# Performance work log

Measured on AMD Instinct MI355X. Metric: run time of the kernel, lower is better.

Reference implementation:

```python
import jax, jax.numpy as jnp
import numpy as np
from jax import lax

RATIO = 0.25
K = 16
EPS = 1e-5
B, N, CX, COUT, CAUX = 16, 4096, 64, 128, 32


def _fps(p, m):
    # Farthest point sampling on one cloud p:(N,3); deterministic start at index 0.
    mind = jnp.sum((p - p[0]) ** 2, axis=-1)  # (N,) min sq-dist to selected set
    def step(mind, _):
        nxt = jnp.argmax(mind)
        d = jnp.sum((p - p[nxt]) ** 2, axis=-1)
        return jnp.minimum(mind, d), nxt
    _, rest = lax.scan(step, mind, None, length=m - 1)
    return jnp.concatenate([jnp.zeros((1,), jnp.int32), rest.astype(jnp.int32)])


def setup_inputs() -> dict:
    key = jax.random.key(0)
    k1, k2, k3, k4, k5, k6 = jax.random.split(key, 6)
    P = B * N
    x = jax.random.normal(k1, (P, CX), jnp.float32)
    pos = jax.random.normal(k2, (P, 3), jnp.float32)
    batch = jnp.repeat(jnp.arange(B, dtype=jnp.int32), N)  # equal-size clouds
    aux = jax.random.normal(k3, (P, CAUX), jnp.float32)
    # MLP params: Linear(CX->COUT) + BatchNorm affine
    W = jax.random.normal(k4, (CX, COUT), jnp.float32) * (1.0 / np.sqrt(CX))
    b = jax.random.normal(k5, (COUT,), jnp.float32) * 0.02
    gamma = jnp.ones((COUT,), jnp.float32) + 0.1 * jax.random.normal(k6, (COUT,), jnp.float32)
    beta = jnp.zeros((COUT,), jnp.float32)
    return {"x": x, "pos": pos, "batch": batch, "aux": aux,
            "W": W, "b": b, "gamma": gamma, "beta": beta}


def reference(x, pos, batch, aux, W, b, gamma, beta):
    P = x.shape[0]
    nb = int(batch[-1]) + 1            # number of clouds (equal-size)
    n = P // nb
    m = int(n * RATIO)                 # clusters per cloud
    pos_b = pos.reshape(nb, n, 3)
    # --- FPS per cloud ---
    idx_local = jax.vmap(lambda p: _fps(p, m))(pos_b)                     # (B, M)
    id_clusters = (idx_local + jnp.arange(nb, dtype=jnp.int32)[:, None] * n).reshape(-1)
    centers = jnp.take_along_axis(pos_b, idx_local[..., None], axis=1)    # (B, M, 3)
    # --- kNN of all points to cluster centers, within each cloud ---
    d2 = jnp.sum((centers[:, :, None, :] - pos_b[:, None, :, :]) ** 2, axis=-1)  # (B, M, N)
    _, nb_local = lax.top_k(-d2, K)                                       # (B, M, K)
    nb_global = (nb_local + jnp.arange(nb, dtype=jnp.int32)[:, None, None] * n).reshape(-1)
    # --- MLP: Linear -> BatchNorm(batch stats, train mode) -> ReLU ---
    h = x @ W + b
    mu = jnp.mean(h, axis=0)
    var = jnp.var(h, axis=0)
    x_trans = jax.nn.relu(gamma * (h - mu) * lax.rsqrt(var + EPS) + beta)  # (P, Cout)
    # --- gather + per-cluster max / mean pooling (== scatter over knn edges) ---
    x_out = jnp.max(x_trans[nb_global].reshape(nb * m, K, -1), axis=1)     # (B*M, Cout)
    aux_out = jnp.mean(aux[nb_global].reshape(nb * m, K, -1), axis=1)      # (B*M, Caux)
    sub_pos = centers.reshape(-1, 3)
    sub_batch = batch[id_clusters]
    return x_out, sub_pos, sub_batch, aux_out, id_clusters
```

## Files before the change

kernel.cpp:

```cpp
#include <hip/hip_runtime.h>
#include <hip/hip_bf16.h>
#include <math.h>

#define NB    16
#define NPC   4096
#define MPC   1024
#define PTOT  65536
#define NCLU  16384
#define KNN_  16
#define CIN   64
#define COUT_ 128
#define CAUX_ 32

#define OFF_XOUT   0
#define OFF_SUBPOS (NCLU*COUT_)
#define OFF_SUBB   (OFF_SUBPOS + NCLU*3)
#define OFF_AUX    (OFF_SUBB + NCLU)
#define OFF_IDCL   (OFF_AUX + NCLU*CAUX_)

#define WS_H        0
#define WS_CENTERS  (PTOT*COUT_*4)
#define WS_STATS    (WS_CENTERS + NCLU*16)
#define WS_NEED     (WS_STATS + 256*4)

#define SM_LX    0
#define SM_LY    16384
#define SM_LZ    32768
#define SM_CAND  49152
#define SM_CSEL  49664
#define SM_SIDX  53760
#define SM_HIST  70144
#define SM_SCANA 72192
#define SM_SCANB 74240
#define SM_XT    0
#define SM_WL    17408
#define SM_BS    50176
#define SM_BQ    50688
#define SM_SIZE  76288

__device__ __forceinline__ double dmax(double a, double b) { return __builtin_fmax(a, b); }
__device__ __forceinline__ double dmin(double a, double b) { return __builtin_fmin(a, b); }
__device__ __forceinline__ double pk(float d, int lo) {
  return __hiloint2double(__float_as_int(d), lo);
}
__device__ __forceinline__ int pk_lo(double k) {
  return (int)(unsigned)(__double_as_longlong(k) & 0xFFFFFFFFll);
}

template <int CTRL>
__device__ __forceinline__ double dpp64(double v) {
  long long u = __double_as_longlong(v);
  int lo = (int)(unsigned)(u & 0xFFFFFFFFll);
  int hi = (int)(unsigned)((unsigned long long)u >> 32);
  int rlo = __builtin_amdgcn_update_dpp(0, lo, CTRL, 0xf, 0xf, true);
  int rhi = __builtin_amdgcn_update_dpp(0, hi, CTRL, 0xf, 0xf, true);
  return __longlong_as_double(((long long)rhi << 32) | (long long)(unsigned)rlo);
}
template <int CTRL>
__device__ __forceinline__ float dpp32(float x) {
  return __int_as_float(__builtin_amdgcn_update_dpp(0, __float_as_int(x), CTRL, 0xf, 0xf, true));
}
#define ROR1 0x121
#define ROR2 0x122
#define ROR4 0x124
#define ROR8 0x128

__device__ __forceinline__ double rowmax16(double w) {
  w = dmax(w, dpp64<ROR1>(w));
  w = dmax(w, dpp64<ROR2>(w));
  w = dmax(w, dpp64<ROR4>(w));
  w = dmax(w, dpp64<ROR8>(w));
  return w;
}
__device__ __forceinline__ float row16maxf(float m) {
  m = fmaxf(m, dpp32<ROR1>(m));
  m = fmaxf(m, dpp32<ROR2>(m));
  m = fmaxf(m, dpp32<ROR4>(m));
  m = fmaxf(m, dpp32<ROR8>(m));
  return m;
}
__device__ __forceinline__ float row16minf(float m) {
  m = fminf(m, dpp32<ROR1>(m));
  m = fminf(m, dpp32<ROR2>(m));
  m = fminf(m, dpp32<ROR4>(m));
  m = fminf(m, dpp32<ROR8>(m));
  return m;
}

__device__ __forceinline__ int mort3(int x, int y, int z) {
  int m = 0;
  #pragma unroll
  for (int bb = 0; bb < 3; ++bb)
    m |= (((x >> bb) & 1) << (3*bb + 2)) | (((y >> bb) & 1) << (3*bb + 1)) |
         (((z >> bb) & 1) << (3*bb));
  return m;
}

__device__ void fps_block(char* smem, const float* __restrict__ pos,
                          float4* __restrict__ centers, float* __restrict__ out)
{
  #pragma clang fp contract(off)
  float* lx = (float*)(smem + SM_LX);
  float* ly = (float*)(smem + SM_LY);
  float* lz = (float*)(smem + SM_LZ);
  double* cand = (double*)(smem + SM_CAND);
  int*   csel = (int*)(smem + SM_CSEL);
  int*   sidx = (int*)(smem + SM_SIDX);
  int*   hist = (int*)(smem + SM_HIST);
  float* bbs  = (float*)(smem + SM_HIST);
  int*   sA   = (int*)(smem + SM_SCANA);
  int*   sB   = (int*)(smem + SM_SCANB);
  const int b = blockIdx.x;
  const int t = threadIdx.x;
  const float* pb = pos + (size_t)b * NPC * 3;
  const int entry  = (t >> 6) * 4 + ((t >> 4) & 3);
  const bool writer = ((t & 15) == 0);

  float ox[8], oy[8], oz[8];
  {
    const float4* src = (const float4*)(pb + t * 24);
    float4 v[6];
    #pragma unroll
    for (int i = 0; i < 6; ++i) v[i] = src[i];
    const float* f = (const float*)v;
    #pragma unroll
    for (int j = 0; j < 8; ++j) {
      ox[j] = f[3*j]; oy[j] = f[3*j+1]; oz[j] = f[3*j+2];
      lx[t*8+j] = ox[j]; ly[t*8+j] = oy[j]; lz[t*8+j] = oz[j];
    }
  }
  float mnx = ox[0], mxx = ox[0], mny = oy[0], mxy = oy[0], mnz = oz[0], mxz = oz[0];
  #pragma unroll
  for (int j = 1; j < 8; ++j) {
    mnx = fminf(mnx, ox[j]); mxx = fmaxf(mxx, ox[j]);
    mny = fminf(mny, oy[j]); mxy = fmaxf(mxy, oy[j]);
    mnz = fminf(mnz, oz[j]); mxz = fmaxf(mxz, oz[j]);
  }
  mnx = row16minf(mnx); mxx = row16maxf(mxx);
  mny = row16minf(mny); mxy = row16maxf(mxy);
  mnz = row16minf(mnz); mxz = row16maxf(mxz);
  if (writer) {
    bbs[entry] = mnx; bbs[32+entry] = mxx; bbs[64+entry]  = mny;
    bbs[96+entry] = mxy; bbs[128+entry] = mnz; bbs[160+entry] = mxz;
  }
  __syncthreads();
  float gx0 = bbs[0], gx1 = bbs[32], gy0 = bbs[64], gy1 = bbs[96], gz0 = bbs[128], gz1 = bbs[160];
  #pragma unroll 8
  for (int w = 1; w < 32; ++w) {
    gx0 = fminf(gx0, bbs[w]);     gx1 = fmaxf(gx1, bbs[32+w]);
    gy0 = fminf(gy0, bbs[64+w]);  gy1 = fmaxf(gy1, bbs[96+w]);
    gz0 = fminf(gz0, bbs[128+w]); gz1 = fmaxf(gz1, bbs[160+w]);
  }
  __syncthreads();
  hist[t] = 0;
  __syncthreads();
  const float scx = 8.0f / ((gx1 - gx0) + 1e-6f);
  const float scy = 8.0f / ((gy1 - gy0) + 1e-6f);
  const float scz = 8.0f / ((gz1 - gz0) + 1e-6f);
  int key[8];
  #pragma unroll
  for (int j = 0; j < 8; ++j) {
    int cx = min(7, max(0, (int)((ox[j] - gx0) * scx)));
    int cy = min(7, max(0, (int)((oy[j] - gy0) * scy)));
    int cz = min(7, max(0, (int)((oz[j] - gz0) * scz)));
    key[j] = mort3(cx, cy, cz);
    atomicAdd(&hist[key[j]], 1);
  }
  __syncthreads();
  const int hv = hist[t];
  sA[t] = hv;
  __syncthreads();
  for (int off = 1; off < 512; off <<= 1) {
    const int o = (t >= off) ? sA[t - off] : 0;
    __syncthreads();
    sA[t] += o;
    __syncthreads();
  }
  sB[t] = sA[t] - hv;
  __syncthreads();
  #pragma unroll
  for (int j = 0; j < 8; ++j) {
    const int slot = atomicAdd(&sB[key[j]], 1);
    sidx[slot] = t*8 + j;
  }
  __syncthreads();
  float px[8], py[8], pz[8], mind[8];
  int lo8[8];
  float bxn = 1e30f, bxx = -1e30f, byn = 1e30f, byy = -1e30f, bzn = 1e30f, bzz = -1e30f;
  #pragma unroll
  for (int j = 0; j < 8; ++j) {
    const int sid = sidx[t*8 + j];
    px[j] = lx[sid]; py[j] = ly[sid]; pz[j] = lz[sid];
    lo8[j] = 4095 - sid;
    bxn = fminf(bxn, px[j]); bxx = fmaxf(bxx, px[j]);
    byn = fminf(byn, py[j]); byy = fmaxf(byy, py[j]);
    bzn = fminf(bzn, pz[j]); bzz = fmaxf(bzz, pz[j]);
  }
  const float x0 = lx[0], y0 = ly[0], z0 = lz[0];
  if (t == 0) csel[0] = 0;

  double bk;
  {
    double k4[4];
    #pragma unroll
    for (int jp = 0; jp < 4; ++jp) {
      const int j0 = 2*jp, j1 = 2*jp + 1;
      float dx0 = px[j0]-x0, dy0 = py[j0]-y0, dz0 = pz[j0]-z0;
      float dx1 = px[j1]-x0, dy1 = py[j1]-y0, dz1 = pz[j1]-z0;
      float d0 = (dx0*dx0 + dy0*dy0) + dz0*dz0;
      float d1 = (dx1*dx1 + dy1*dy1) + dz1*dz1;
      mind[j0] = d0; mind[j1] = d1;
      k4[jp] = dmax(pk(d0, lo8[j0]), pk(d1, lo8[j1]));
    }
    bk = dmax(dmax(k4[0], k4[1]), dmax(k4[2], k4[3]));
  }

  for (int s = 1; s < MPC; ++s) {
    double w = rowmax16(bk);
    const int ph = (s & 1) * 32;
    if (writer) cand[ph + entry] = w;
    __syncthreads();
    double2 pr = ((const double2*)(cand + ph))[t & 15];
    double w2 = rowmax16(dmax(pr.x, pr.y));
    const int sel = 4095 - pk_lo(w2);
    const float sx = lx[sel], sy = ly[sel], sz = lz[sel];
    if (t == 0) csel[s] = sel;
    const float bkhi = __int_as_float(__double2hiint(bk));
    const float cxd = fmaxf(fmaxf(bxn - sx, sx - bxx), 0.0f);
    const float cyd = fmaxf(fmaxf(byn - sy, sy - byy), 0.0f);
    const float czd = fmaxf(fmaxf(bzn - sz, sz - bzz), 0.0f);
    const float lb = 0.99f * ((cxd*cxd + cyd*cyd) + czd*czd);
    if (lb < bkhi) {
      double k4[4];
      #pragma unroll
      for (int jp = 0; jp < 4; ++jp) {
        const int j0 = 2*jp, j1 = 2*jp + 1;
        float dx0 = px[j0]-sx, dy0 = py[j0]-sy, dz0 = pz[j0]-sz;
        float dx1 = px[j1]-sx, dy1 = py[j1]-sy, dz1 = pz[j1]-sz;
        float d0 = (dx0*dx0 + dy0*dy0) + dz0*dz0;
        float d1 = (dx1*dx1 + dy1*dy1) + dz1*dz1;
        float m0 = fminf(mind[j0], d0), m1 = fminf(mind[j1], d1);
        mind[j0] = m0; mind[j1] = m1;
        k4[jp] = dmax(pk(m0, lo8[j0]), pk(m1, lo8[j1]));
      }
      bk = dmax(dmax(k4[0], k4[1]), dmax(k4[2], k4[3]));
    }
  }
  __syncthreads();
  for (int c = t; c < MPC; c += 512) {
    const int il = csel[c];
    const int cl = b*MPC + c;
    const float X = lx[il], Y = ly[il], Z = lz[il];
    centers[cl] = make_float4(X, Y, Z, 0.0f);
    out[OFF_SUBPOS + cl*3 + 0] = X;
    out[OFF_SUBPOS + cl*3 + 1] = Y;
    out[OFF_SUBPOS + cl*3 + 2] = Z;
    out[OFF_SUBB + cl] = (float)b;
    out[OFF_IDCL + cl] = (float)(b*NPC + il);
  }
}

__device__ void gemm_block(char* smem, const float* __restrict__ x,
                           const float* __restrict__ W, const float* __restrict__ bias,
                           float* __restrict__ h, float* __restrict__ stats, int blk)
{
  float (*xT)[68]  = (float(*)[68])(smem + SM_XT);
  float (*Wl)[128] = (float(*)[128])(smem + SM_WL);
  float* bsum = (float*)(smem + SM_BS);
  float* bsq  = (float*)(smem + SM_BQ);
  const int t = threadIdx.x;
  const int row0 = blk * 64;
  if (t < 128) { bsum[t] = 0.0f; bsq[t] = 0.0f; }
  #pragma unroll
  for (int i = 0; i < 8; ++i) {
    const int idx = t + i*512;
    xT[idx & 63][idx >> 6] = x[(size_t)row0*64 + idx];
  }
  #pragma unroll
  for (int i = 0; i < 16; ++i) {
    const int idx = t + i*512;
    ((float*)Wl)[idx] = W[idx];
  }
  __syncthreads();
  const int tx = t & 31, ty = t >> 5;
  float acc[4][4] = {};
  #pragma unroll 8
  for (int k = 0; k < 64; ++k) {
    const float4 a  = *(const float4*)&xT[k][ty*4];
    const float4 b0 = *(const float4*)&Wl[k][tx*4];
    const float av[4] = {a.x, a.y, a.z, a.w};
    const float bw[4] = {b0.x, b0.y, b0.z, b0.w};
    #pragma unroll
    for (int i2 = 0; i2 < 4; ++i2)
      #pragma unroll
      for (int e = 0; e < 4; ++e)
        acc[i2][e] += av[i2] * bw[e];
  }
  const int c0 = tx*4;
  float bb[4];
  #pragma unroll
  for (int e = 0; e < 4; ++e) bb[e] = bias[c0+e];
  float s4[4] = {}, q4[4] = {};
  #pragma unroll
  for (int i2 = 0; i2 < 4; ++i2) {
    float vv[4];
    #pragma unroll
    for (int e = 0; e < 4; ++e) {
      float v = acc[i2][e] + bb[e];
      vv[e] = v; s4[e] += v; q4[e] += v*v;
    }
    const int r = row0 + ty*4 + i2;
    *(float4*)&h[(size_t)r*128 + c0] = make_float4(vv[0], vv[1], vv[2], vv[3]);
  }
  #pragma unroll
  for (int e = 0; e < 4; ++e) {
    atomicAdd(&bsum[c0+e], s4[e]);
    atomicAdd(&bsq[c0+e],  q4[e]);
  }
  __syncthreads();
  if (t < 128) {
    atomicAdd(&stats[t],      bsum[t]);
    atomicAdd(&stats[128+t],  bsq[t]);
  }
}

__global__ __launch_bounds__(512) void fused_fps_gemm(const float* __restrict__ pos,
                                                      float4* __restrict__ centers,
                                                      float* __restrict__ out,
                                                      const float* __restrict__ x,
                                                      const float* __restrict__ W,
                                                      const float* __restrict__ bias,
                                                      float* __restrict__ h,
                                                      float* __restrict__ stats)
{
  __shared__ __align__(16) char smem[SM_SIZE];
  if (blockIdx.x < NB) fps_block(smem, pos, centers, out);
  else                 gemm_block(smem, x, W, bias, h, stats, blockIdx.x - NB);
}

#define KBIG __hiloint2double(0x7f7fffff, 0xffffffff)
#define CD_STRIDE 17

#define KP_CD    0
#define KP_SCL   69632
#define KP_SSH   70144
#define KP_FID   70656
#define KP_SIZE  72704

__global__ __launch_bounds__(512) void knn_pool(const float* __restrict__ pos,
                                                const float4* __restrict__ centers,
                                                const float* __restrict__ h,
                                                const float* __restrict__ aux,
                                                const float* __restrict__ stats,
                                                const float* __restrict__ gamma,
                                                const float* __restrict__ beta,
                                                float* __restrict__ out)
{
  #pragma clang fp contract(off)
  __shared__ __align__(16) char sm2[KP_SIZE];
  float4* lp = (float4*)(sm2);
  double* cd = (double*)(sm2 + KP_CD);
  float*  scl = (float*)(sm2 + KP_SCL);
  float*  ssh = (float*)(sm2 + KP_SSH);
  int*    fid = (int*)(sm2 + KP_FID);
  const int vblk = ((blockIdx.x & 7) << 6) | (blockIdx.x >> 3);
  const int b   = vblk >> 5;
  const int c0  = (vblk & 31) * 32;
  const int t   = threadIdx.x;
  const int q   = t & 15;
  const int cc  = t >> 4;
  if (t < 128) {
    const float inv = 1.0f / 65536.0f;
    const float mu  = stats[t] * inv;
    const float var = stats[128+t] * inv - mu*mu;
    const float sc  = gamma[t] * rsqrtf(var + 1e-5f);
    scl[t] = sc;
    ssh[t] = beta[t] - mu*sc;
  }
  const float* pb = pos + (size_t)b * NPC * 3;
  for (int i = t; i < NPC; i += 512)
    lp[i] = make_float4(pb[3*i], pb[3*i+1], pb[3*i+2], 0.0f);
  __syncthreads();
  const float4 C = centers[b*MPC + c0 + cc];
  double L[16];
  #pragma unroll
  for (int k = 0; k < 16; ++k) L[k] = KBIG;
  for (int jj = 0; jj < NPC/16; ++jj) {
    const int j = jj*16 + q;
    const float4 p = lp[j];
    float dx = C.x - p.x, dy = C.y - p.y, dz = C.z - p.z;
    float d2 = (dx*dx + dy*dy) + dz*dz;
    double nk = pk(d2, j);
    if (nk < L[0]) {
      #pragma unroll
      for (int k = 0; k < 15; ++k) L[k] = dmin(L[k], dmax(L[k+1], nk));
      L[15] = dmin(L[15], nk);
    }
  }
  __syncthreads();
  #pragma unroll
  for (int k = 0; k < 16; ++k) cd[t*CD_STRIDE + k] = L[k];
  __syncthreads();
  if (q < 4) {
    #pragma unroll
    for (int r = 1; r <= 3; ++r) {
      const double* src = cd + (cc*16 + q + 4*r)*CD_STRIDE;
      #pragma unroll
      for (int k = 0; k < 16; ++k) {
        double nk = src[k];
        if (nk < L[0]) {
          #pragma unroll
          for (int m = 0; m < 15; ++m) L[m] = dmin(L[m], dmax(L[m+1], nk));
          L[15] = dmin(L[15], nk);
        }
      }
    }
    #pragma unroll
    for (int k = 0; k < 16; ++k) cd[t*CD_STRIDE + k] = L[k];
  }
  __syncthreads();
  if (q == 0) {
    #pragma unroll
    for (int r = 1; r <= 3; ++r) {
      const double* src = cd + (cc*16 + r)*CD_STRIDE;
      #pragma unroll
      for (int k = 0; k < 16; ++k) {
        double nk = src[k];
        if (nk < L[0]) {
          #pragma unroll
          for (int m = 0; m < 15; ++m) L[m] = dmin(L[m], dmax(L[m+1], nk));
          L[15] = dmin(L[15], nk);
        }
      }
    }
    #pragma unroll
    for (int k = 0; k < 16; ++k) fid[cc*16 + k] = b*NPC + pk_lo(L[k]);
  }
  __syncthreads();
  for (int g = 0; g < 8; ++g) {
    const int cc2 = g*4 + (t >> 7);
    const int col = t & 127;
    const int cl  = b*MPC + c0 + cc2;
    const float sc = scl[col], sh = ssh[col];
    float mv = 0.0f;
    #pragma unroll
    for (int k = 0; k < 16; ++k) {
      const float hv = h[(size_t)fid[cc2*16 + k]*128 + col];
      mv = fmaxf(mv, fmaxf(sc*hv + sh, 0.0f));
    }
    out[OFF_XOUT + (size_t)cl*128 + col] = mv;
    if (col < 32) {
      float s = 0.0f;
      #pragma unroll
      for (int k = 0; k < 16; ++k) s += aux[(size_t)fid[cc2*16 + k]*32 + col];
      out[OFF_AUX + (size_t)cl*32 + col] = s * (1.0f/16.0f);
    }
  }
}

extern "C" void kernel_launch(void* const* d_in, const int* in_sizes, int n_in,
                              void* d_out, int out_size, void* d_ws, size_t ws_size,
                              hipStream_t stream)
{
  const float* x     = (const float*)d_in[0];
  const float* pos   = (const float*)d_in[1];
  const float* aux   = (const float*)d_in[3];
  const float* W     = (const float*)d_in[4];
  const float* bias  = (const float*)d_in[5];
  const float* gamma = (const float*)d_in[6];
  const float* beta  = (const float*)d_in[7];
  float* out = (float*)d_out;
  char*  ws  = (char*)d_ws;
  if (ws_size < (size_t)WS_NEED) return;

  float*  h       = (float*)(ws + WS_H);
  float4* centers = (float4*)(ws + WS_CENTERS);
  float*  stats   = (float*)(ws + WS_STATS);

  hipMemsetAsync(stats, 0, 256*4, stream);
  hipLaunchKernelGGL(fused_fps_gemm, dim3(NB + PTOT/64), dim3(512), 0, stream,
                     pos, centers, out, x, W, bias, h, stats);
  hipLaunchKernelGGL(knn_pool, dim3(512), dim3(512), 0, stream,
                     pos, centers, h, aux, stats, gamma, beta, out);
}
```

Before: 734.3 us.

## Fuse FPS, GEMM and kNN-pool into one persistent kernel with progress flags

Replaces the two-kernel launch with a persistent kernel. Sixteen blocks run FPS per cloud and publish center batches every 32 selections through a progress flag. The other blocks first pull GEMM tiles from an atomic work queue, then pull kNN work items split into four point-slices per 32-center chunk. Partial top-16 lists are merged in global memory under a per-chunk spinlock, and the last slice does the BN/max/mean pooling once all GEMM tiles are done. This overlaps the serial FPS tail with the GEMM and kNN work, at the cost of spin-waits, lock contention, and a reliance on all blocks being co-resident to avoid deadlock.

```diff
diff --git a/kernel.cpp b/kernel.cpp
--- a/kernel.cpp
+++ b/kernel.cpp
@@ -20,8 +20,19 @@
 
 #define WS_H        0
 #define WS_CENTERS  (PTOT*COUT_*4)
-#define WS_STATS    (WS_CENTERS + NCLU*16)
-#define WS_NEED     (WS_STATS + 256*4)
+#define WS_LISTS    (WS_CENTERS + NCLU*16)
+#define WS_STATS    (WS_LISTS + NCLU*KNN_*8)
+#define WS_FLAGS    (WS_STATS + 1024)
+#define FL_GEMM   0
+#define FL_WORK   1
+#define FL_GWORK  2
+#define FL_PROG   3
+#define FL_CNT    19
+#define FL_LOCK   531
+#define FL_CHUNK  1043
+#define FL_TOTAL  1555
+#define WS_NEED_MEGA ((size_t)WS_FLAGS + 4u*FL_TOTAL)
+#define WS_NEED_LEG  ((size_t)WS_STATS + 1024)
 
 #define SM_LX    0
 #define SM_LY    16384
@@ -32,11 +43,16 @@
 #define SM_HIST  70144
 #define SM_SCANA 72192
 #define SM_SCANB 74240
+#define SM_SIZE  76288
 #define SM_XT    0
 #define SM_WL    17408
 #define SM_BS    50176
 #define SM_BQ    50688
-#define SM_SIZE  76288
+#define KP_CD    0
+#define KP_SCL   69632
+#define KP_SSH   70144
+#define KP_FID   70656
+#define KP_FLAG  72704
 
 __device__ __forceinline__ double dmax(double a, double b) { return __builtin_fmax(a, b); }
 __device__ __forceinline__ double dmin(double a, double b) { return __builtin_fmin(a, b); }
@@ -46,7 +62,6 @@
 __device__ __forceinline__ int pk_lo(double k) {
   return (int)(unsigned)(__double_as_longlong(k) & 0xFFFFFFFFll);
 }
-
 template <int CTRL>
 __device__ __forceinline__ double dpp64(double v) {
   long long u = __double_as_longlong(v);
@@ -64,29 +79,21 @@
 #define ROR2 0x122
 #define ROR4 0x124
 #define ROR8 0x128
-
 __device__ __forceinline__ double rowmax16(double w) {
-  w = dmax(w, dpp64<ROR1>(w));
-  w = dmax(w, dpp64<ROR2>(w));
-  w = dmax(w, dpp64<ROR4>(w));
-  w = dmax(w, dpp64<ROR8>(w));
+  w = dmax(w, dpp64<ROR1>(w)); w = dmax(w, dpp64<ROR2>(w));
+  w = dmax(w, dpp64<ROR4>(w)); w = dmax(w, dpp64<ROR8>(w));
   return w;
 }
 __device__ __forceinline__ float row16maxf(float m) {
-  m = fmaxf(m, dpp32<ROR1>(m));
-  m = fmaxf(m, dpp32<ROR2>(m));
-  m = fmaxf(m, dpp32<ROR4>(m));
-  m = fmaxf(m, dpp32<ROR8>(m));
+  m = fmaxf(m, dpp32<ROR1>(m)); m = fmaxf(m, dpp32<ROR2>(m));
+  m = fmaxf(m, dpp32<ROR4>(m)); m = fmaxf(m, dpp32<ROR8>(m));
   return m;
 }
 __device__ __forceinline__ float row16minf(float m) {
-  m = fminf(m, dpp32<ROR1>(m));
-  m = fminf(m, dpp32<ROR2>(m));
-  m = fminf(m, dpp32<ROR4>(m));
-  m = fminf(m, dpp32<ROR8>(m));
+  m = fminf(m, dpp32<ROR1>(m)); m = fminf(m, dpp32<ROR2>(m));
+  m = fminf(m, dpp32<ROR4>(m)); m = fminf(m, dpp32<ROR8>(m));
   return m;
 }
-
 __device__ __forceinline__ int mort3(int x, int y, int z) {
   int m = 0;
   #pragma unroll
@@ -96,8 +103,17 @@
   return m;
 }
 
+#define INS16(Lr, nk) do { \
+  _Pragma("unroll") \
+  for (int _m = 0; _m < 15; ++_m) Lr[_m] = dmin(Lr[_m], dmax(Lr[_m+1], (nk))); \
+  Lr[15] = dmin(Lr[15], (nk)); } while (0)
+
+#define KBIG __hiloint2double(0x7f7fffff, 0xffffffff)
+#define CD_STRIDE 17
+
 __device__ void fps_block(char* smem, const float* __restrict__ pos,
-                          float4* __restrict__ centers, float* __restrict__ out)
+                          float4* __restrict__ centers, float* __restrict__ out,
+                          int* prog)
 {
   #pragma clang fp contract(off)
   float* lx = (float*)(smem + SM_LX);
@@ -198,7 +214,6 @@
   }
   const float x0 = lx[0], y0 = ly[0], z0 = lz[0];
   if (t == 0) csel[0] = 0;
-
   double bk;
   {
     double k4[4];
@@ -220,6 +235,22 @@
     const int ph = (s & 1) * 32;
     if (writer) cand[ph + entry] = w;
     __syncthreads();
+    if ((s & 31) == 0) {
+      if (t < 32) {
+        const int fc = s - 32 + t;
+        const int il = csel[fc];
+        const int cl = b*MPC + fc;
+        const float X = lx[il], Y = ly[il], Z = lz[il];
+        centers[cl] = make_float4(X, Y, Z, 0.0f);
+        out[OFF_SUBPOS + cl*3 + 0] = X;
+        out[OFF_SUBPOS + cl*3 + 1] = Y;
+        out[OFF_SUBPOS + cl*3 + 2] = Z;
+        out[OFF_SUBB + cl] = (float)b;
+        out[OFF_IDCL + cl] = (float)(b*NPC + il);
+      }
+      __syncthreads();
+      if (prog && t == 0) { __threadfence(); atomicExch(&prog[b], s); }
+    }
     double2 pr = ((const double2*)(cand + ph))[t & 15];
     double w2 = rowmax16(dmax(pr.x, pr.y));
     const int sel = 4095 - pk_lo(w2);
@@ -247,9 +278,10 @@
     }
   }
   __syncthreads();
-  for (int c = t; c < MPC; c += 512) {
-    const int il = csel[c];
-    const int cl = b*MPC + c;
+  if (t < 32) {
+    const int fc = 992 + t;
+    const int il = csel[fc];
+    const int cl = b*MPC + fc;
     const float X = lx[il], Y = ly[il], Z = lz[il];
     centers[cl] = make_float4(X, Y, Z, 0.0f);
     out[OFF_SUBPOS + cl*3 + 0] = X;
@@ -258,11 +290,13 @@
     out[OFF_SUBB + cl] = (float)b;
     out[OFF_IDCL + cl] = (float)(b*NPC + il);
   }
-}
-
-__device__ void gemm_block(char* smem, const float* __restrict__ x,
-                           const float* __restrict__ W, const float* __restrict__ bias,
-                           float* __restrict__ h, float* __restrict__ stats, int blk)
+  __syncthreads();
+  if (prog && t == 0) { __threadfence(); atomicExch(&prog[b], MPC); }
+}
+
+__device__ void gemm_tile(char* smem, const float* __restrict__ x,
+                          const float* __restrict__ W, const float* __restrict__ bias,
+                          float* __restrict__ h, float* __restrict__ stats, int blk)
 {
   float (*xT)[68]  = (float(*)[68])(smem + SM_XT);
   float (*Wl)[128] = (float(*)[128])(smem + SM_WL);
@@ -321,6 +355,175 @@
   if (t < 128) {
     atomicAdd(&stats[t],      bsum[t]);
     atomicAdd(&stats[128+t],  bsq[t]);
+  }
+  __syncthreads();
+}
+
+__global__ __launch_bounds__(512, 4)
+void mega2(const float* __restrict__ pos, float4* __restrict__ centers,
+           float* __restrict__ out, const float* __restrict__ x,
+           const float* __restrict__ W, const float* __restrict__ bias,
+           float* __restrict__ h, float* __restrict__ stats,
+           double* __restrict__ lists, int* __restrict__ flags,
+           const float* __restrict__ gamma, const float* __restrict__ beta,
+           const float* __restrict__ aux)
+{
+  #pragma clang fp contract(off)
+  __shared__ __align__(16) char smem[SM_SIZE];
+  const int t = threadIdx.x;
+  int* sfl = (int*)(smem + KP_FLAG);
+  if (blockIdx.x < NB) {
+    fps_block(smem, pos, centers, out, flags + FL_PROG);
+    return;
+  }
+  for (;;) {
+    __syncthreads();
+    if (t == 0) sfl[0] = atomicAdd(&flags[FL_GWORK], 1);
+    __syncthreads();
+    const int gid = sfl[0];
+    if (gid >= 1024) break;
+    gemm_tile(smem, x, W, bias, h, stats, gid);
+    if (t == 0) { __threadfence(); atomicAdd(&flags[FL_GEMM], 1); }
+  }
+  double* cd  = (double*)(smem + KP_CD);
+  float*  scl = (float*)(smem + KP_SCL);
+  float*  ssh = (float*)(smem + KP_SSH);
+  int*    fid = (int*)(smem + KP_FID);
+  const int q  = t & 15;
+  const int cc = t >> 4;
+  for (;;) {
+    __syncthreads();
+    if (t == 0) sfl[0] = atomicAdd(&flags[FL_WORK], 1);
+    __syncthreads();
+    const int id = sfl[0];
+    if (id >= 2048) break;
+    const int slice   = id & 3;
+    const int chunkid = id >> 2;
+    const int cloud   = chunkid & 15;
+    const int cidx    = chunkid >> 4;
+    const int c0      = cidx * 32;
+    if (t == 0) {
+      while (atomicAdd(&flags[FL_PROG + cloud], 0) < c0 + 32)
+        __builtin_amdgcn_s_sleep(32);
+    }
+    __syncthreads();
+    __threadfence();
+    float4* mpos = (float4*)smem;
+    {
+      const float* pb = pos + ((size_t)cloud * NPC + slice * 1024) * 3;
+      for (int i = t; i < 1024; i += 512)
+        mpos[i] = make_float4(pb[3*i], pb[3*i+1], pb[3*i+2], 0.0f);
+    }
+    __syncthreads();
+    const float4 C = centers[cloud*MPC + c0 + cc];
+    double L[16];
+    #pragma unroll
+    for (int k = 0; k < 16; ++k) L[k] = KBIG;
+    for (int jj = 0; jj < 64; ++jj) {
+      const int jl = jj*16 + q;
+      const float4 p = mpos[jl];
+      float dx = C.x - p.x, dy = C.y - p.y, dz = C.z - p.z;
+      float d2 = (dx*dx + dy*dy) + dz*dz;
+      double nk = pk(d2, slice*1024 + jl);
+      if (nk < L[0]) INS16(L, nk);
+    }
+    __syncthreads();
+    #pragma unroll
+    for (int k = 0; k < 16; ++k) cd[t*CD_STRIDE + k] = L[k];
+    __syncthreads();
+    if (q < 4) {
+      #pragma unroll
+      for (int r = 1; r <= 3; ++r) {
+        const double* src = cd + (cc*16 + q + 4*r)*CD_STRIDE;
+        #pragma unroll
+        for (int k = 0; k < 16; ++k) {
+          double nk = src[k];
+          if (nk < L[0]) INS16(L, nk);
+        }
+      }
+      #pragma unroll
+      for (int k = 0; k < 16; ++k) cd[t*CD_STRIDE + k] = L[k];
+    }
+    __syncthreads();
+    if (q == 0) {
+      #pragma unroll
+      for (int r = 1; r <= 3; ++r) {
+        const double* src = cd + (cc*16 + r)*CD_STRIDE;
+        #pragma unroll
+        for (int k = 0; k < 16; ++k) {
+          double nk = src[k];
+          if (nk < L[0]) INS16(L, nk);
+        }
+      }
+    }
+    if (t == 0) {
+      while (atomicCAS(&flags[FL_LOCK + chunkid], 0, 1) != 0)
+        __builtin_amdgcn_s_sleep(8);
+    }
+    __syncthreads();
+    __threadfence();
+    if (q == 0) {
+      double* gl = lists + (size_t)(cloud*MPC + c0 + cc) * 16;
+      if (atomicAdd(&flags[FL_CNT + chunkid], 0) != 0) {
+        #pragma unroll
+        for (int k = 0; k < 16; ++k) {
+          double nk = gl[k];
+          if (nk < L[0]) INS16(L, nk);
+        }
+      }
+      #pragma unroll
+      for (int k = 0; k < 16; ++k) gl[k] = L[k];
+    }
+    __threadfence();
+    __syncthreads();
+    if (t == 0) {
+      atomicExch(&flags[FL_CNT + chunkid], 1);
+      __threadfence();
+      atomicExch(&flags[FL_LOCK + chunkid], 0);
+      const int dn = atomicAdd(&flags[FL_CHUNK + chunkid], 1);
+      sfl[1] = (dn == 3) ? 1 : 0;
+    }
+    __syncthreads();
+    if (sfl[1]) {
+      if (t == 0) {
+        while (atomicAdd(&flags[FL_GEMM], 0) < 1024)
+          __builtin_amdgcn_s_sleep(32);
+      }
+      __syncthreads();
+      __threadfence();
+      if (t < 128) {
+        const float inv = 1.0f / 65536.0f;
+        const float mu  = stats[t] * inv;
+        const float var = stats[128+t] * inv - mu*mu;
+        const float sc  = gamma[t] * rsqrtf(var + 1e-5f);
+        scl[t] = sc;
+        ssh[t] = beta[t] - mu*sc;
+      }
+      {
+        const int g = cloud*MPC + c0 + (t >> 4);
+        fid[t] = cloud*NPC + pk_lo(lists[(size_t)g*16 + (t & 15)]);
+      }
+      __syncthreads();
+      for (int g2 = 0; g2 < 8; ++g2) {
+        const int cc2 = g2*4 + (t >> 7);
+        const int col = t & 127;
+        const int cl  = cloud*MPC + c0 + cc2;
+        const float sc = scl[col], sh = ssh[col];
+        float mv = 0.0f;
+        #pragma unroll
+        for (int k = 0; k < 16; ++k) {
+          const float hv = h[(size_t)fid[cc2*16 + k]*128 + col];
+          mv = fmaxf(mv, fmaxf(sc*hv + sh, 0.0f));
+        }
+        out[OFF_XOUT + (size_t)cl*128 + col] = mv;
+        if (col < 32) {
+          float s = 0.0f;
+          #pragma unroll
+          for (int k = 0; k < 16; ++k) s += aux[(size_t)fid[cc2*16 + k]*32 + col];
+          out[OFF_AUX + (size_t)cl*32 + col] = s * (1.0f/16.0f);
+        }
+      }
+    }
   }
 }
 
@@ -334,18 +537,9 @@
                                                       float* __restrict__ stats)
 {
   __shared__ __align__(16) char smem[SM_SIZE];
-  if (blockIdx.x < NB) fps_block(smem, pos, centers, out);
-  else                 gemm_block(smem, x, W, bias, h, stats, blockIdx.x - NB);
-}
-
-#define KBIG __hiloint2double(0x7f7fffff, 0xffffffff)
-#define CD_STRIDE 17
-
-#define KP_CD    0
-#define KP_SCL   69632
-#define KP_SSH   70144
-#define KP_FID   70656
-#define KP_SIZE  72704
+  if (blockIdx.x < NB) fps_block(smem, pos, centers, out, nullptr);
+  else                 gemm_tile(smem, x, W, bias, h, stats, blockIdx.x - NB);
+}
 
 __global__ __launch_bounds__(512) void knn_pool(const float* __restrict__ pos,
                                                 const float4* __restrict__ centers,
@@ -357,7 +551,7 @@
                                                 float* __restrict__ out)
 {
   #pragma clang fp contract(off)
-  __shared__ __align__(16) char sm2[KP_SIZE];
+  __shared__ __align__(16) char sm2[76288];
   float4* lp = (float4*)(sm2);
   double* cd = (double*)(sm2 + KP_CD);
   float*  scl = (float*)(sm2 + KP_SCL);
@@ -391,11 +585,7 @@
     float dx = C.x - p.x, dy = C.y - p.y, dz = C.z - p.z;
     float d2 = (dx*dx + dy*dy) + dz*dz;
     double nk = pk(d2, j);
-    if (nk < L[0]) {
-      #pragma unroll
-      for (int k = 0; k < 15; ++k) L[k] = dmin(L[k], dmax(L[k+1], nk));
-      L[15] = dmin(L[15], nk);
-    }
+    if (nk < L[0]) INS16(L, nk);
   }
   __syncthreads();
   #pragma unroll
@@ -408,11 +598,7 @@
       #pragma unroll
       for (int k = 0; k < 16; ++k) {
         double nk = src[k];
-        if (nk < L[0]) {
-          #pragma unroll
-          for (int m = 0; m < 15; ++m) L[m] = dmin(L[m], dmax(L[m+1], nk));
-          L[15] = dmin(L[15], nk);
-        }
+        if (nk < L[0]) INS16(L, nk);
       }
     }
     #pragma unroll
@@ -426,11 +612,7 @@
       #pragma unroll
       for (int k = 0; k < 16; ++k) {
         double nk = src[k];
-        if (nk < L[0]) {
-          #pragma unroll
-          for (int m = 0; m < 15; ++m) L[m] = dmin(L[m], dmax(L[m+1], nk));
-          L[15] = dmin(L[15], nk);
-        }
+        if (nk < L[0]) INS16(L, nk);
       }
     }
     #pragma unroll
@@ -471,15 +653,24 @@
   const float* beta  = (const float*)d_in[7];
   float* out = (float*)d_out;
   char*  ws  = (char*)d_ws;
-  if (ws_size < (size_t)WS_NEED) return;
+  if (ws_size < WS_NEED_LEG) return;
 
   float*  h       = (float*)(ws + WS_H);
   float4* centers = (float4*)(ws + WS_CENTERS);
+  double* lists   = (double*)(ws + WS_LISTS);
   float*  stats   = (float*)(ws + WS_STATS);
-
-  hipMemsetAsync(stats, 0, 256*4, stream);
-  hipLaunchKernelGGL(fused_fps_gemm, dim3(NB + PTOT/64), dim3(512), 0, stream,
-                     pos, centers, out, x, W, bias, h, stats);
-  hipLaunchKernelGGL(knn_pool, dim3(512), dim3(512), 0, stream,
-                     pos, centers, h, aux, stats, gamma, beta, out);
-}
+  int*    flags   = (int*)(ws + WS_FLAGS);
+
+  if (ws_size >= WS_NEED_MEGA) {
+    hipMemsetAsync(stats, 0, 1024 + 4*FL_TOTAL, stream);
+    hipLaunchKernelGGL(mega2, dim3(512), dim3(512), 0, stream,
+                       pos, centers, out, x, W, bias, h, stats,
+                       lists, flags, gamma, beta, aux);
+  } else {
+    hipMemsetAsync(stats, 0, 1024, stream);
+    hipLaunchKernelGGL(fused_fps_gemm, dim3(NB + PTOT/64), dim3(512), 0, stream,
+                       pos, centers, out, x, W, bias, h, stats);
+    hipLaunchKernelGGL(knn_pool, dim3(512), dim3(512), 0, stream,
+                       pos, centers, h, aux, stats, gamma, beta, out);
+  }
+}
```

Result: slower. 1.384 ms (+88.5%).
